# Kernel tuning notes

Measured on AMD Instinct MI355X. Metric: run time of the kernel, lower is better.

The kernel has to match this reference:

```python
import jax, jax.numpy as jnp
import numpy as np

EPS = 1e-5

def layer_norm(x, g, b):
    mu = jnp.mean(x, axis=-1, keepdims=True)
    var = jnp.var(x, axis=-1, keepdims=True)
    return (x - mu) * jax.lax.rsqrt(var + EPS) * g + b

def setup_inputs() -> dict:
    key = jax.random.key(0)
    ks = jax.random.split(key, 9)
    B, S, E = 16, 2048, 512
    H = 2 * E
    q = jax.random.normal(ks[0], (B, S, E), dtype=jnp.float32)
    k = jax.random.normal(ks[1], (B, S, E), dtype=jnp.float32)
    v = jax.random.normal(ks[2], (B, S, E), dtype=jnp.float32)
    # LayerNorm params (norm1 and norm3; norm2 is dead code in the original)
    ln1_g = jnp.ones((E,), jnp.float32); ln1_b = jnp.zeros((E,), jnp.float32)
    ln3_g = jnp.ones((E,), jnp.float32); ln3_b = jnp.zeros((E,), jnp.float32)
    # FFN params, torch Linear default init (uniform +- 1/sqrt(fan_in))
    lim1 = 1.0 / np.sqrt(E)
    w1 = jax.random.uniform(ks[3], (E, H), jnp.float32, -lim1, lim1)
    b1 = jax.random.uniform(ks[4], (H,), jnp.float32, -lim1, lim1)
    lim2 = 1.0 / np.sqrt(H)
    w2 = jax.random.uniform(ks[5], (H, E), jnp.float32, -lim2, lim2)
    b2 = jax.random.uniform(ks[6], (E,), jnp.float32, -lim2, lim2)
    return {"q": q, "k": k, "v": v, "ln1_g": ln1_g, "ln1_b": ln1_b,
            "w1": w1, "b1": b1, "w2": w2, "b2": b2,
            "ln3_g": ln3_g, "ln3_b": ln3_b}

def reference(q, k, v, ln1_g, ln1_b, w1, b1, w2, b2, ln3_g, ln3_b):
    # single-head full attention: scores [B,S,S]
    scale = 1.0 / jnp.sqrt(jnp.asarray(q.shape[-1], q.dtype))
    scores = jnp.einsum('bse,bte->bst', q, k) * scale
    attn = jax.nn.softmax(scores, axis=-1)
    attn_out = jnp.einsum('bst,bte->bse', attn, v)
    # residual + LayerNorm (dropout is identity at p=0 / eval)
    x = layer_norm(q + attn_out, ln1_g, ln1_b)
    # FFN: Linear -> exact GELU -> Linear
    h = jax.nn.gelu(jnp.einsum('bse,eh->bsh', x, w1) + b1, approximate=False)
    ff = jnp.einsum('bsh,he->bse', h, w2) + b2
    return layer_norm(x + ff, ln3_g, ln3_b)
```

## Files before the change

kernel.cpp:

```cpp
#include <hip/hip_runtime.h>
#include <cstdint>

#define B_ 16
#define S_ 2048
#define E_ 512
#define H_ 1024
#define SCALE 0.044194173824159216f

typedef __attribute__((ext_vector_type(8))) short short8;
typedef __attribute__((ext_vector_type(4))) float floatx4;

static __device__ __forceinline__ unsigned short f2bf(float f) {
    unsigned u = __float_as_uint(f);
    u = u + 0x7FFFu + ((u >> 16) & 1u);
    return (unsigned short)(u >> 16);
}
static __device__ __forceinline__ float bf2f(unsigned short h) {
    return __uint_as_float(((unsigned)h) << 16);
}

__global__ void cvt_f32_bf16(const float* __restrict__ in, unsigned short* __restrict__ out, int n8) {
    int i = blockIdx.x * blockDim.x + threadIdx.x;
    if (i >= n8) return;
    const float4* p = (const float4*)in + (long)i * 2;
    float4 a = p[0], b = p[1];
    union { unsigned short u[8]; uint4 v; } r;
    r.u[0] = f2bf(a.x); r.u[1] = f2bf(a.y); r.u[2] = f2bf(a.z); r.u[3] = f2bf(a.w);
    r.u[4] = f2bf(b.x); r.u[5] = f2bf(b.y); r.u[6] = f2bf(b.z); r.u[7] = f2bf(b.w);
    ((uint4*)out)[i] = r.v;
}

__global__ void transpose_cvt(const float* __restrict__ in, unsigned short* __restrict__ out,
                              int R, int C, long inBS, long outBS) {
    __shared__ float t[64 * 68];
    const int z = blockIdx.z;
    in += (long)z * inBS; out += (long)z * outBS;
    const int c0 = blockIdx.x * 64, r0 = blockIdx.y * 64;
    const int tid = threadIdx.x;
    {
        int col4 = (tid & 15) * 4;
        #pragma unroll
        for (int i = 0; i < 4; i++) {
            int row = (tid >> 4) + i * 16;
            float4 v = *(const float4*)(in + (long)(r0 + row) * C + c0 + col4);
            *(float4*)(&t[row * 68 + col4]) = v;
        }
    }
    __syncthreads();
    {
        int oc = tid >> 2;
        int ob = (tid & 3) * 16;
        union { unsigned short u[16]; uint4 v[2]; } r;
        #pragma unroll
        for (int j = 0; j < 16; j++) r.u[j] = f2bf(t[(ob + j) * 68 + oc]);
        uint4* dst = (uint4*)(out + (long)(c0 + oc) * R + r0 + ob);
        dst[0] = r.v[0]; dst[1] = r.v[1];
    }
}

__launch_bounds__(256, 2)
__global__ void attn_kernel(const float* __restrict__ q,
                            const unsigned short* __restrict__ kb,
                            const unsigned short* __restrict__ vt,
                            const float* __restrict__ g1,
                            const float* __restrict__ bb1,
                            unsigned short* __restrict__ xb) {
    __shared__ unsigned short pLDS[64 * 72];
    __shared__ float aLDS[64];
    __shared__ float lLDS[64];
    __shared__ float sumLDS[64 * 4];
    __shared__ float sqLDS[64 * 4];
    const int tid = threadIdx.x;
    const int w = tid >> 6, lane = tid & 63, quad = lane >> 4, l16 = lane & 15;
    const int b = blockIdx.x >> 5, q0 = (blockIdx.x & 31) * 64;

    short8 aq[16];
    {
        const float* qp = q + (long)(b * S_ + q0 + 16 * w + l16) * E_ + quad * 8;
        #pragma unroll
        for (int kc = 0; kc < 16; kc++) {
            float4 x0 = *(const float4*)(qp + kc * 32);
            float4 x1 = *(const float4*)(qp + kc * 32 + 4);
            short8 t;
            t[0] = (short)f2bf(x0.x); t[1] = (short)f2bf(x0.y);
            t[2] = (short)f2bf(x0.z); t[3] = (short)f2bf(x0.w);
            t[4] = (short)f2bf(x1.x); t[5] = (short)f2bf(x1.y);
            t[6] = (short)f2bf(x1.z); t[7] = (short)f2bf(x1.w);
            aq[kc] = t;
        }
    }

    floatx4 oacc[4][8];
    const floatx4 zf = {0.f, 0.f, 0.f, 0.f};
    #pragma unroll
    for (int qg = 0; qg < 4; qg++)
        #pragma unroll
        for (int nt = 0; nt < 8; nt++) oacc[qg][nt] = zf;
    float m_[4] = {-INFINITY, -INFINITY, -INFINITY, -INFINITY};
    float l_[4] = {0.f, 0.f, 0.f, 0.f};

    const unsigned short* kbase = kb + (long)(b * S_ + l16) * E_ + quad * 8;
    const unsigned short* vbase = vt + (long)(b * E_ + 128 * w + l16) * S_ + quad * 8;

    for (int t = 0; t < 32; t++) {
        const int kt0 = t * 64;
        floatx4 sacc[4] = {zf, zf, zf, zf};
        const unsigned short* kt = kbase + (long)kt0 * E_;
        #pragma unroll
        for (int kc = 0; kc < 16; kc++) {
            short8 b0 = *(const short8*)(kt + 0 * 16 * E_ + kc * 32);
            short8 b1 = *(const short8*)(kt + 1 * 16 * E_ + kc * 32);
            short8 b2 = *(const short8*)(kt + 2 * 16 * E_ + kc * 32);
            short8 b3 = *(const short8*)(kt + 3 * 16 * E_ + kc * 32);
            sacc[0] = __builtin_amdgcn_mfma_f32_16x16x32_bf16(aq[kc], b0, sacc[0], 0, 0, 0);
            sacc[1] = __builtin_amdgcn_mfma_f32_16x16x32_bf16(aq[kc], b1, sacc[1], 0, 0, 0);
            sacc[2] = __builtin_amdgcn_mfma_f32_16x16x32_bf16(aq[kc], b2, sacc[2], 0, 0, 0);
            sacc[3] = __builtin_amdgcn_mfma_f32_16x16x32_bf16(aq[kc], b3, sacc[3], 0, 0, 0);
        }
        float rm[4], al[4], P[4][4], rs[4];
        #pragma unroll
        for (int r = 0; r < 4; r++)
            rm[r] = fmaxf(fmaxf(sacc[0][r], sacc[1][r]), fmaxf(sacc[2][r], sacc[3][r])) * SCALE;
        #pragma unroll
        for (int off = 1; off < 16; off <<= 1)
            #pragma unroll
            for (int r = 0; r < 4; r++) rm[r] = fmaxf(rm[r], __shfl_xor(rm[r], off));
        #pragma unroll
        for (int r = 0; r < 4; r++) {
            float mn = fmaxf(m_[r], rm[r]);
            al[r] = __expf(m_[r] - mn);
            m_[r] = mn;
            float p0 = __expf(sacc[0][r] * SCALE - mn);
            float p1 = __expf(sacc[1][r] * SCALE - mn);
            float p2 = __expf(sacc[2][r] * SCALE - mn);
            float p3 = __expf(sacc[3][r] * SCALE - mn);
            P[0][r] = p0; P[1][r] = p1; P[2][r] = p2; P[3][r] = p3;
            rs[r] = (p0 + p1) + (p2 + p3);
        }
        #pragma unroll
        for (int off = 1; off < 16; off <<= 1)
            #pragma unroll
            for (int r = 0; r < 4; r++) rs[r] += __shfl_xor(rs[r], off);
        #pragma unroll
        for (int r = 0; r < 4; r++) l_[r] = l_[r] * al[r] + rs[r];
        #pragma unroll
        for (int nt = 0; nt < 4; nt++)
            #pragma unroll
            for (int r = 0; r < 4; r++)
                pLDS[(16 * w + quad * 4 + r) * 72 + nt * 16 + l16] = f2bf(P[nt][r]);
        if (l16 == 0) {
            #pragma unroll
            for (int r = 0; r < 4; r++) aLDS[16 * w + quad * 4 + r] = al[r];
        }
        __syncthreads();
        short8 pf[4][2];
        #pragma unroll
        for (int qg = 0; qg < 4; qg++)
            #pragma unroll
            for (int kc = 0; kc < 2; kc++)
                pf[qg][kc] = *(const short8*)(&pLDS[(qg * 16 + l16) * 72 + kc * 32 + quad * 8]);
        float av[4][4];
        #pragma unroll
        for (int qg = 0; qg < 4; qg++)
            #pragma unroll
            for (int r = 0; r < 4; r++) av[qg][r] = aLDS[qg * 16 + quad * 4 + r];
        #pragma unroll
        for (int qg = 0; qg < 4; qg++)
            #pragma unroll
            for (int nt = 0; nt < 8; nt++)
                #pragma unroll
                for (int r = 0; r < 4; r++) oacc[qg][nt][r] *= av[qg][r];
        const unsigned short* vtt = vbase + kt0;
        #pragma unroll
        for (int nt = 0; nt < 8; nt++) {
            short8 vf0 = *(const short8*)(vtt + (long)nt * 16 * S_);
            short8 vf1 = *(const short8*)(vtt + (long)nt * 16 * S_ + 32);
            #pragma unroll
            for (int qg = 0; qg < 4; qg++) {
                oacc[qg][nt] = __builtin_amdgcn_mfma_f32_16x16x32_bf16(pf[qg][0], vf0, oacc[qg][nt], 0, 0, 0);
                oacc[qg][nt] = __builtin_amdgcn_mfma_f32_16x16x32_bf16(pf[qg][1], vf1, oacc[qg][nt], 0, 0, 0);
            }
        }
        __syncthreads();
    }
    if (l16 == 0) {
        #pragma unroll
        for (int r = 0; r < 4; r++) lLDS[16 * w + quad * 4 + r] = l_[r];
    }
    __syncthreads();
    float lv[4][4];
    #pragma unroll
    for (int qg = 0; qg < 4; qg++)
        #pragma unroll
        for (int r = 0; r < 4; r++) lv[qg][r] = 1.f / lLDS[qg * 16 + quad * 4 + r];
    float ps[4][4], pq2[4][4];
    #pragma unroll
    for (int qg = 0; qg < 4; qg++)
        #pragma unroll
        for (int r = 0; r < 4; r++) { ps[qg][r] = 0.f; pq2[qg][r] = 0.f; }
    #pragma unroll
    for (int qg = 0; qg < 4; qg++)
        #pragma unroll
        for (int nt = 0; nt < 8; nt++)
            #pragma unroll
            for (int r = 0; r < 4; r++) {
                int qrow = q0 + qg * 16 + quad * 4 + r;
                int feat = 128 * w + nt * 16 + l16;
                float y = q[(long)(b * S_ + qrow) * E_ + feat] + oacc[qg][nt][r] * lv[qg][r];
                oacc[qg][nt][r] = y;
                ps[qg][r] += y; pq2[qg][r] += y * y;
            }
    #pragma unroll
    for (int off = 1; off < 16; off <<= 1)
        #pragma unroll
        for (int qg = 0; qg < 4; qg++)
            #pragma unroll
            for (int r = 0; r < 4; r++) {
                ps[qg][r] += __shfl_xor(ps[qg][r], off);
                pq2[qg][r] += __shfl_xor(pq2[qg][r], off);
            }
    if (l16 == 0) {
        #pragma unroll
        for (int qg = 0; qg < 4; qg++)
            #pragma unroll
            for (int r = 0; r < 4; r++) {
                int row = qg * 16 + quad * 4 + r;
                sumLDS[row * 4 + w] = ps[qg][r];
                sqLDS[row * 4 + w] = pq2[qg][r];
            }
    }
    __syncthreads();
    float mu[4][4], rstd[4][4];
    #pragma unroll
    for (int qg = 0; qg < 4; qg++)
        #pragma unroll
        for (int r = 0; r < 4; r++) {
            int row = qg * 16 + quad * 4 + r;
            float s = (sumLDS[row * 4 + 0] + sumLDS[row * 4 + 1]) + (sumLDS[row * 4 + 2] + sumLDS[row * 4 + 3]);
            float s2 = (sqLDS[row * 4 + 0] + sqLDS[row * 4 + 1]) + (sqLDS[row * 4 + 2] + sqLDS[row * 4 + 3]);
            float mean = s * (1.f / E_);
            float var = s2 * (1.f / E_) - mean * mean;
            mu[qg][r] = mean;
            rstd[qg][r] = rsqrtf(fmaxf(var, 0.f) + 1e-5f);
        }
    float gv[8], bv[8];
    #pragma unroll
    for (int nt = 0; nt < 8; nt++) {
        int feat = 128 * w + nt * 16 + l16;
        gv[nt] = g1[feat]; bv[nt] = bb1[feat];
    }
    #pragma unroll
    for (int qg = 0; qg < 4; qg++)
        #pragma unroll
        for (int nt = 0; nt < 8; nt++)
            #pragma unroll
            for (int r = 0; r < 4; r++) {
                int qrow = q0 + qg * 16 + quad * 4 + r;
                int feat = 128 * w + nt * 16 + l16;
                xb[(long)(b * S_ + qrow) * E_ + feat] =
                    f2bf((oacc[qg][nt][r] - mu[qg][r]) * rstd[qg][r] * gv[nt] + bv[nt]);
            }
}

__launch_bounds__(256)
__global__ void gemm1_kernel(const unsigned short* __restrict__ A,
                             const unsigned short* __restrict__ Bt,
                             const float* __restrict__ bias,
                             unsigned short* __restrict__ Out) {
    __shared__ unsigned short ldsA[128 * 72], ldsB[128 * 72];
    const int tid = threadIdx.x, w = tid >> 6, lane = tid & 63, quad = lane >> 4, l16 = lane & 15;
    const int nb = blockIdx.x & 7, mbi = blockIdx.x >> 3;
    const long m0 = (long)mbi * 128; const int n0 = nb * 128;
    const int wm = (w >> 1) * 64, wn = (w & 1) * 64;
    const floatx4 zf = {0.f, 0.f, 0.f, 0.f};
    floatx4 acc[4][4];
    #pragma unroll
    for (int i = 0; i < 4; i++)
        #pragma unroll
        for (int j = 0; j < 4; j++) acc[i][j] = zf;
    for (int k0 = 0; k0 < 512; k0 += 64) {
        #pragma unroll
        for (int i = 0; i < 4; i++) {
            int cid = i * 256 + tid;
            int row = cid >> 3, c8 = (cid & 7) * 8;
            *(short8*)(&ldsA[row * 72 + c8]) = *(const short8*)(A + (m0 + row) * 512 + k0 + c8);
            *(short8*)(&ldsB[row * 72 + c8]) = *(const short8*)(Bt + (long)(n0 + row) * 512 + k0 + c8);
        }
        __syncthreads();
        #pragma unroll
        for (int kc = 0; kc < 2; kc++) {
            short8 af[4], bf[4];
            #pragma unroll
            for (int mt = 0; mt < 4; mt++)
                af[mt] = *(const short8*)(&ldsA[(wm + mt * 16 + l16) * 72 + kc * 32 + quad * 8]);
            #pragma unroll
            for (int nt = 0; nt < 4; nt++)
                bf[nt] = *(const short8*)(&ldsB[(wn + nt * 16 + l16) * 72 + kc * 32 + quad * 8]);
            #pragma unroll
            for (int mt = 0; mt < 4; mt++)
                #pragma unroll
                for (int nt = 0; nt < 4; nt++)
                    acc[mt][nt] = __builtin_amdgcn_mfma_f32_16x16x32_bf16(af[mt], bf[nt], acc[mt][nt], 0, 0, 0);
        }
        __syncthreads();
    }
    #pragma unroll
    for (int nt = 0; nt < 4; nt++) {
        int n = n0 + wn + nt * 16 + l16;
        float bv = bias[n];
        #pragma unroll
        for (int mt = 0; mt < 4; mt++) {
            long m = m0 + wm + mt * 16 + quad * 4;
            #pragma unroll
            for (int r = 0; r < 4; r++) {
                float v = acc[mt][nt][r] + bv;
                v = 0.5f * v * (1.f + erff(v * 0.70710678118f));
                Out[(m + r) * H_ + n] = f2bf(v);
            }
        }
    }
}

__launch_bounds__(256, 2)
__global__ void gemm2_ln3_kernel(const unsigned short* __restrict__ A,
                                 const unsigned short* __restrict__ Bt,
                                 const float* __restrict__ bias,
                                 const unsigned short* __restrict__ resid,
                                 const float* __restrict__ g3, const float* __restrict__ bb3,
                                 float* __restrict__ Out) {
    __shared__ unsigned short ldsA[64 * 40], ldsB[512 * 40];
    __shared__ float sumLDS[64 * 4], sqLDS[64 * 4];
    const int tid = threadIdx.x, w = tid >> 6, lane = tid & 63, quad = lane >> 4, l16 = lane & 15;
    const long m0 = (long)blockIdx.x * 64;
    const floatx4 zf = {0.f, 0.f, 0.f, 0.f};
    floatx4 acc[4][8];
    #pragma unroll
    for (int i = 0; i < 4; i++)
        #pragma unroll
        for (int j = 0; j < 8; j++) acc[i][j] = zf;
    for (int k0 = 0; k0 < 1024; k0 += 32) {
        {
            int row = tid >> 2, c8 = (tid & 3) * 8;
            *(short8*)(&ldsA[row * 40 + c8]) = *(const short8*)(A + (m0 + row) * 1024 + k0 + c8);
        }
        #pragma unroll
        for (int i = 0; i < 8; i++) {
            int cid = i * 256 + tid;
            int row = cid >> 2, c8 = (cid & 3) * 8;
            *(short8*)(&ldsB[row * 40 + c8]) = *(const short8*)(Bt + (long)row * 1024 + k0 + c8);
        }
        __syncthreads();
        short8 af[4], bf[8];
        #pragma unroll
        for (int mt = 0; mt < 4; mt++)
            af[mt] = *(const short8*)(&ldsA[(mt * 16 + l16) * 40 + quad * 8]);
        #pragma unroll
        for (int nt = 0; nt < 8; nt++)
            bf[nt] = *(const short8*)(&ldsB[(128 * w + nt * 16 + l16) * 40 + quad * 8]);
        #pragma unroll
        for (int mt = 0; mt < 4; mt++)
            #pragma unroll
            for (int nt = 0; nt < 8; nt++)
                acc[mt][nt] = __builtin_amdgcn_mfma_f32_16x16x32_bf16(af[mt], bf[nt], acc[mt][nt], 0, 0, 0);
        __syncthreads();
    }
    float ps[4][4], pq2[4][4];
    #pragma unroll
    for (int mt = 0; mt < 4; mt++)
        #pragma unroll
        for (int r = 0; r < 4; r++) { ps[mt][r] = 0.f; pq2[mt][r] = 0.f; }
    #pragma unroll
    for (int nt = 0; nt < 8; nt++) {
        int n = 128 * w + nt * 16 + l16;
        float bv = bias[n];
        #pragma unroll
        for (int mt = 0; mt < 4; mt++) {
            long m = m0 + mt * 16 + quad * 4;
            #pragma unroll
            for (int r = 0; r < 4; r++) {
                float v = acc[mt][nt][r] + bv + bf2f(resid[(m + r) * E_ + n]);
                acc[mt][nt][r] = v;
                ps[mt][r] += v; pq2[mt][r] += v * v;
            }
        }
    }
    #pragma unroll
    for (int off = 1; off < 16; off <<= 1)
        #pragma unroll
        for (int mt = 0; mt < 4; mt++)
            #pragma unroll
            for (int r = 0; r < 4; r++) {
                ps[mt][r] += __shfl_xor(ps[mt][r], off);
                pq2[mt][r] += __shfl_xor(pq2[mt][r], off);
            }
    if (l16 == 0) {
        #pragma unroll
        for (int mt = 0; mt < 4; mt++)
            #pragma unroll
            for (int r = 0; r < 4; r++) {
                int row = mt * 16 + quad * 4 + r;
                sumLDS[row * 4 + w] = ps[mt][r];
                sqLDS[row * 4 + w] = pq2[mt][r];
            }
    }
    __syncthreads();
    float mu[4][4], rstd[4][4];
    #pragma unroll
    for (int mt = 0; mt < 4; mt++)
        #pragma unroll
        for (int r = 0; r < 4; r++) {
            int row = mt * 16 + quad * 4 + r;
            float s = (sumLDS[row * 4 + 0] + sumLDS[row * 4 + 1]) + (sumLDS[row * 4 + 2] + sumLDS[row * 4 + 3]);
            float s2 = (sqLDS[row * 4 + 0] + sqLDS[row * 4 + 1]) + (sqLDS[row * 4 + 2] + sqLDS[row * 4 + 3]);
            float mean = s * (1.f / E_);
            float var = s2 * (1.f / E_) - mean * mean;
            mu[mt][r] = mean;
            rstd[mt][r] = rsqrtf(fmaxf(var, 0.f) + 1e-5f);
        }
    float gv[8], bv3[8];
    #pragma unroll
    for (int nt = 0; nt < 8; nt++) {
        int n = 128 * w + nt * 16 + l16;
        gv[nt] = g3[n]; bv3[nt] = bb3[n];
    }
    #pragma unroll
    for (int nt = 0; nt < 8; nt++) {
        int n = 128 * w + nt * 16 + l16;
        #pragma unroll
        for (int mt = 0; mt < 4; mt++) {
            long m = m0 + mt * 16 + quad * 4;
            #pragma unroll
            for (int r = 0; r < 4; r++)
                Out[(m + r) * E_ + n] =
                    (acc[mt][nt][r] - mu[mt][r]) * rstd[mt][r] * gv[nt] + bv3[nt];
        }
    }
}

extern "C" void kernel_launch(void* const* d_in, const int* in_sizes, int n_in,
                              void* d_out, int out_size, void* d_ws, size_t ws_size,
                              hipStream_t stream) {
    const float* q    = (const float*)d_in[0];
    const float* k    = (const float*)d_in[1];
    const float* v    = (const float*)d_in[2];
    const float* ln1g = (const float*)d_in[3];
    const float* ln1b = (const float*)d_in[4];
    const float* w1   = (const float*)d_in[5];
    const float* b1   = (const float*)d_in[6];
    const float* w2   = (const float*)d_in[7];
    const float* b2   = (const float*)d_in[8];
    const float* ln3g = (const float*)d_in[9];
    const float* ln3b = (const float*)d_in[10];

    char* ws = (char*)d_ws;
    unsigned short* kb  = (unsigned short*)(ws);
    unsigned short* vt  = (unsigned short*)(ws + 33554432);
    unsigned short* h   = (unsigned short*)(ws);
    unsigned short* xb  = (unsigned short*)(ws + 67108864);
    unsigned short* w1t = (unsigned short*)(ws + 100663296);
    unsigned short* w2t = (unsigned short*)(ws + 101711872);
    float* ob = (float*)d_out;

    cvt_f32_bf16<<<8192, 256, 0, stream>>>(k, kb, 2097152);
    transpose_cvt<<<dim3(8, 32, 16), 256, 0, stream>>>(v, vt, 2048, 512, (long)2048 * 512, (long)512 * 2048);
    transpose_cvt<<<dim3(16, 8, 1), 256, 0, stream>>>(w1, w1t, 512, 1024, 0, 0);
    transpose_cvt<<<dim3(8, 16, 1), 256, 0, stream>>>(w2, w2t, 1024, 512, 0, 0);
    attn_kernel<<<512, 256, 0, stream>>>(q, kb, vt, ln1g, ln1b, xb);
    gemm1_kernel<<<2048, 256, 0, stream>>>(xb, w1t, b1, h);
    gemm2_ln3_kernel<<<512, 256, 0, stream>>>(h, w2t, b2, xb, ln3g, ln3b, ob);
}
```

Before: 992.5 us.

## Double-buffer K tiles in LDS via async global_load_lds with swizzle

The attention kernel now stages K tiles of 32 rows into a double-buffered, XOR-swizzled LDS buffer using global_load_lds, prefetching the next tile while computing the current one. Before, every wave read K directly from global memory. The KV tile shrinks from 64 to 32, so there are twice as many loop iterations, each with two barriers, and the P buffer is smaller. The 64KB of K staging in LDS may lower occupancy below the 2 blocks per CU launch bound, and there is no explicit wait on the async loads beyond __syncthreads.

Result: faster. 810.5 us (-18.3%).

```diff
diff --git a/kernel.cpp b/kernel.cpp
--- a/kernel.cpp
+++ b/kernel.cpp
@@ -6,6 +6,8 @@
 #define E_ 512
 #define H_ 1024
 #define SCALE 0.044194173824159216f
+#define KVB 32
+#define NTILES 64
 
 typedef __attribute__((ext_vector_type(8))) short short8;
 typedef __attribute__((ext_vector_type(4))) float floatx4;
@@ -65,7 +67,8 @@
                             const float* __restrict__ g1,
                             const float* __restrict__ bb1,
                             unsigned short* __restrict__ xb) {
-    __shared__ unsigned short pLDS[64 * 72];
+    __shared__ unsigned short kLDS[2][KVB * E_];
+    __shared__ unsigned short pLDS[64 * 40];
     __shared__ float aLDS[64];
     __shared__ float lLDS[64];
     __shared__ float sumLDS[64 * 4];
@@ -73,6 +76,9 @@
     const int tid = threadIdx.x;
     const int w = tid >> 6, lane = tid & 63, quad = lane >> 4, l16 = lane & 15;
     const int b = blockIdx.x >> 5, q0 = (blockIdx.x & 31) * 64;
+    const floatx4 zf = {0.f, 0.f, 0.f, 0.f};
+
+    const unsigned short* kb_b = kb + (long)b * S_ * E_;
 
     short8 aq[16];
     {
@@ -91,7 +97,6 @@
     }
 
     floatx4 oacc[4][8];
-    const floatx4 zf = {0.f, 0.f, 0.f, 0.f};
     #pragma unroll
     for (int qg = 0; qg < 4; qg++)
         #pragma unroll
@@ -99,28 +104,52 @@
     float m_[4] = {-INFINITY, -INFINITY, -INFINITY, -INFINITY};
     float l_[4] = {0.f, 0.f, 0.f, 0.f};
 
-    const unsigned short* kbase = kb + (long)(b * S_ + l16) * E_ + quad * 8;
     const unsigned short* vbase = vt + (long)(b * E_ + 128 * w + l16) * S_ + quad * 8;
 
-    for (int t = 0; t < 32; t++) {
-        const int kt0 = t * 64;
-        floatx4 sacc[4] = {zf, zf, zf, zf};
-        const unsigned short* kt = kbase + (long)kt0 * E_;
+    {
+        #pragma unroll
+        for (int j = 0; j < 8; j++) {
+            int row = j * 4 + w;
+            const unsigned short* g = kb_b + (long)row * E_ + ((lane * 8) ^ ((row & 7) << 3));
+            __builtin_amdgcn_global_load_lds(
+                (const __attribute__((address_space(1))) void*)g,
+                (__attribute__((address_space(3))) void*)(&kLDS[0][row * E_]), 16, 0, 0);
+        }
+    }
+    __syncthreads();
+
+    for (int t = 0; t < NTILES; t++) {
+        const int cur = t & 1;
+        const int kt0 = t * KVB;
+
+        if (t + 1 < NTILES) {
+            const unsigned short* kb_t = kb_b + (long)(kt0 + KVB) * E_;
+            #pragma unroll
+            for (int j = 0; j < 8; j++) {
+                int row = j * 4 + w;
+                const unsigned short* g = kb_t + (long)row * E_ + ((lane * 8) ^ ((row & 7) << 3));
+                __builtin_amdgcn_global_load_lds(
+                    (const __attribute__((address_space(1))) void*)g,
+                    (__attribute__((address_space(3))) void*)(&kLDS[cur ^ 1][row * E_]), 16, 0, 0);
+            }
+        }
+
+        floatx4 sacc[2] = {zf, zf};
+        const unsigned short* kl = &kLDS[cur][0];
+        const int swz = (l16 & 7) << 3;
         #pragma unroll
         for (int kc = 0; kc < 16; kc++) {
-            short8 b0 = *(const short8*)(kt + 0 * 16 * E_ + kc * 32);
-            short8 b1 = *(const short8*)(kt + 1 * 16 * E_ + kc * 32);
-            short8 b2 = *(const short8*)(kt + 2 * 16 * E_ + kc * 32);
-            short8 b3 = *(const short8*)(kt + 3 * 16 * E_ + kc * 32);
+            const int cx = (kc * 32 + quad * 8) ^ swz;
+            short8 b0 = *(const short8*)(kl + l16 * E_ + cx);
+            short8 b1 = *(const short8*)(kl + (16 + l16) * E_ + cx);
             sacc[0] = __builtin_amdgcn_mfma_f32_16x16x32_bf16(aq[kc], b0, sacc[0], 0, 0, 0);
             sacc[1] = __builtin_amdgcn_mfma_f32_16x16x32_bf16(aq[kc], b1, sacc[1], 0, 0, 0);
-            sacc[2] = __builtin_amdgcn_mfma_f32_16x16x32_bf16(aq[kc], b2, sacc[2], 0, 0, 0);
-            sacc[3] = __builtin_amdgcn_mfma_f32_16x16x32_bf16(aq[kc], b3, sacc[3], 0, 0, 0);
-        }
-        float rm[4], al[4], P[4][4], rs[4];
+        }
+
+        float rm[4], al[4], P2[2][4], rs[4];
         #pragma unroll
         for (int r = 0; r < 4; r++)
-            rm[r] = fmaxf(fmaxf(sacc[0][r], sacc[1][r]), fmaxf(sacc[2][r], sacc[3][r])) * SCALE;
+            rm[r] = fmaxf(sacc[0][r], sacc[1][r]) * SCALE;
         #pragma unroll
         for (int off = 1; off < 16; off <<= 1)
             #pragma unroll
@@ -132,10 +161,8 @@
             m_[r] = mn;
             float p0 = __expf(sacc[0][r] * SCALE - mn);
             float p1 = __expf(sacc[1][r] * SCALE - mn);
-            float p2 = __expf(sacc[2][r] * SCALE - mn);
-            float p3 = __expf(sacc[3][r] * SCALE - mn);
-            P[0][r] = p0; P[1][r] = p1; P[2][r] = p2; P[3][r] = p3;
-            rs[r] = (p0 + p1) + (p2 + p3);
+            P2[0][r] = p0; P2[1][r] = p1;
+            rs[r] = p0 + p1;
         }
         #pragma unroll
         for (int off = 1; off < 16; off <<= 1)
@@ -144,21 +171,20 @@
         #pragma unroll
         for (int r = 0; r < 4; r++) l_[r] = l_[r] * al[r] + rs[r];
         #pragma unroll
-        for (int nt = 0; nt < 4; nt++)
+        for (int nt = 0; nt < 2; nt++)
             #pragma unroll
             for (int r = 0; r < 4; r++)
-                pLDS[(16 * w + quad * 4 + r) * 72 + nt * 16 + l16] = f2bf(P[nt][r]);
+                pLDS[(16 * w + quad * 4 + r) * 40 + nt * 16 + l16] = f2bf(P2[nt][r]);
         if (l16 == 0) {
             #pragma unroll
             for (int r = 0; r < 4; r++) aLDS[16 * w + quad * 4 + r] = al[r];
         }
         __syncthreads();
-        short8 pf[4][2];
+
+        short8 pf[4];
         #pragma unroll
         for (int qg = 0; qg < 4; qg++)
-            #pragma unroll
-            for (int kc = 0; kc < 2; kc++)
-                pf[qg][kc] = *(const short8*)(&pLDS[(qg * 16 + l16) * 72 + kc * 32 + quad * 8]);
+            pf[qg] = *(const short8*)(&pLDS[(qg * 16 + l16) * 40 + quad * 8]);
         float av[4][4];
         #pragma unroll
         for (int qg = 0; qg < 4; qg++)
@@ -173,16 +199,14 @@
         const unsigned short* vtt = vbase + kt0;
         #pragma unroll
         for (int nt = 0; nt < 8; nt++) {
-            short8 vf0 = *(const short8*)(vtt + (long)nt * 16 * S_);
-            short8 vf1 = *(const short8*)(vtt + (long)nt * 16 * S_ + 32);
-            #pragma unroll
-            for (int qg = 0; qg < 4; qg++) {
-                oacc[qg][nt] = __builtin_amdgcn_mfma_f32_16x16x32_bf16(pf[qg][0], vf0, oacc[qg][nt], 0, 0, 0);
-                oacc[qg][nt] = __builtin_amdgcn_mfma_f32_16x16x32_bf16(pf[qg][1], vf1, oacc[qg][nt], 0, 0, 0);
-            }
-        }
-        __syncthreads();
-    }
+            short8 vf = *(const short8*)(vtt + (long)nt * 16 * S_);
+            #pragma unroll
+            for (int qg = 0; qg < 4; qg++)
+                oacc[qg][nt] = __builtin_amdgcn_mfma_f32_16x16x32_bf16(pf[qg], vf, oacc[qg][nt], 0, 0, 0);
+        }
+        __syncthreads();
+    }
+
     if (l16 == 0) {
         #pragma unroll
         for (int r = 0; r < 4; r++) lLDS[16 * w + quad * 4 + r] = l_[r];
```
